# Optimization experiments

Hardware: AMD Instinct MI355X
Metric: run time of the kernel (lower is better)

Reference implementation:

```python
import jax, jax.numpy as jnp
import numpy as np

BETA = 1.0  # nn.SmoothL1Loss() default; module's self.beta=0.5 is never used


def smooth_l1(d):
    ad = jnp.abs(d)
    return jnp.where(ad < BETA, 0.5 * d * d / BETA, ad - 0.5 * BETA)


def setup_inputs() -> dict:
    key = jax.random.key(0)
    k1, k2, k3 = jax.random.split(key, 3)
    B, T, D = 32, 2048, 512
    preds = jax.random.normal(k1, (B, T, D), dtype=jnp.float32)
    targets = jax.random.normal(k2, (B, T, D), dtype=jnp.float32)
    # lengths in [1, T], sorted descending (pack_padded_sequence convention)
    decode_lengths = jnp.sort(jax.random.randint(k3, (B,), 1, T + 1))[::-1]
    return {"preds": preds, "targets": targets, "decode_lengths": decode_lengths}


def reference(preds, targets, decode_lengths):
    B, T, D = preds.shape
    mask = (jnp.arange(T)[None, :] < decode_lengths[:, None]).astype(preds.dtype)  # [B,T]
    lens = decode_lengths.astype(preds.dtype)[:, None]  # [B,1]

    # sentence loss: SmoothL1 between per-sample time-means, mean over D, summed over B
    pred_mean = jnp.einsum('btd,bt->bd', preds, mask) / lens
    targ_mean = jnp.einsum('btd,bt->bd', targets, mask) / lens
    sentence_loss = jnp.sum(jnp.mean(smooth_l1(pred_mean - targ_mean), axis=1))

    # word loss: SmoothL1 over all valid (packed) elements, mean reduction
    elem = smooth_l1(preds - targets) * mask[:, :, None]
    n_valid = jnp.sum(decode_lengths).astype(preds.dtype) * D
    word_loss = jnp.sum(elem) / n_valid

    return word_loss + sentence_loss / B
```

## Files before the change

kernel.cpp:

```cpp
#include <hip/hip_runtime.h>


#define BATCH 32
#define TLEN  2048
#define DDIM  512
#define ROWS  32
#define NCHUNK (TLEN / ROWS)
#define P1_THREADS 128

__device__ __forceinline__ float sl1(float d) {
    float ad = fabsf(d);
    return ad < 1.0f ? 0.5f * d * d : ad - 0.5f;
}

__global__ __launch_bounds__(P1_THREADS)
void pass1(const float* __restrict__ preds, const float* __restrict__ targs,
           const int* __restrict__ lens,
           float* __restrict__ partp,
           float* __restrict__ partt,
           float* __restrict__ wpart)
{
    const int b     = blockIdx.x;
    const int chunk = blockIdx.y;
    const int len   = lens[b];
    const int t0    = chunk * ROWS;
    if (t0 >= len) return;
    const int t1 = min(t0 + ROWS, len);

    const float4* __restrict__ p4 = (const float4*)(preds + (size_t)b * TLEN * DDIM);
    const float4* __restrict__ q4 = (const float4*)(targs + (size_t)b * TLEN * DDIM);
    const int lane4 = threadIdx.x;

    float4 sp = make_float4(0.f, 0.f, 0.f, 0.f);
    float4 st = make_float4(0.f, 0.f, 0.f, 0.f);
    float  w  = 0.f;

    for (int t = t0; t < t1; ++t) {
        float4 p = p4[(size_t)t * (DDIM / 4) + lane4];
        float4 q = q4[(size_t)t * (DDIM / 4) + lane4];
        sp.x += p.x; sp.y += p.y; sp.z += p.z; sp.w += p.w;
        st.x += q.x; st.y += q.y; st.z += q.z; st.w += q.w;
        w += sl1(p.x - q.x) + sl1(p.y - q.y) + sl1(p.z - q.z) + sl1(p.w - q.w);
    }

    float4* op = (float4*)(partp + ((size_t)b * NCHUNK + chunk) * DDIM);
    float4* ot = (float4*)(partt + ((size_t)b * NCHUNK + chunk) * DDIM);
    op[lane4] = sp;
    ot[lane4] = st;

    #pragma unroll
    for (int off = 32; off; off >>= 1) w += __shfl_down(w, off);
    __shared__ float ws[P1_THREADS / 64];
    if ((threadIdx.x & 63) == 0) ws[threadIdx.x >> 6] = w;
    __syncthreads();
    if (threadIdx.x == 0) wpart[b * NCHUNK + chunk] = ws[0] + ws[1];
}

__global__ __launch_bounds__(1024)
void pass2(const float* __restrict__ partp, const float* __restrict__ partt,
           const int* __restrict__ lens, const float* __restrict__ wpart,
           float* __restrict__ out)
{
    const int tid = threadIdx.x;

    float s = 0.f;
    for (int i = tid; i < BATCH * (DDIM / 4); i += 1024) {
        const int b   = i >> 7;
        const int d4  = i & 127;
        const int len = lens[b];
        const int nch = (len + ROWS - 1) / ROWS;
        const float4* pp = (const float4*)(partp + (size_t)b * NCHUNK * DDIM) + d4;
        const float4* tt = (const float4*)(partt + (size_t)b * NCHUNK * DDIM) + d4;
        float4 cp = make_float4(0.f, 0.f, 0.f, 0.f);
        float4 ct = make_float4(0.f, 0.f, 0.f, 0.f);
        for (int c = 0; c < nch; ++c) {
            float4 a  = pp[(size_t)c * (DDIM / 4)];
            float4 bb = tt[(size_t)c * (DDIM / 4)];
            cp.x += a.x; cp.y += a.y; cp.z += a.z; cp.w += a.w;
            ct.x += bb.x; ct.y += bb.y; ct.z += bb.z; ct.w += bb.w;
        }
        const float invL = 1.f / (float)len;
        s += sl1((cp.x - ct.x) * invL) + sl1((cp.y - ct.y) * invL)
           + sl1((cp.z - ct.z) * invL) + sl1((cp.w - ct.w) * invL);
    }

    float wsum = 0.f;
    for (int i = tid; i < BATCH * NCHUNK; i += 1024) {
        const int b = i >> 6;
        const int c = i & (NCHUNK - 1);
        if (c * ROWS < lens[b]) wsum += wpart[i];
    }

    #pragma unroll
    for (int off = 32; off; off >>= 1) {
        s    += __shfl_down(s, off);
        wsum += __shfl_down(wsum, off);
    }
    __shared__ float rs[16], rw[16];
    if ((tid & 63) == 0) { rs[tid >> 6] = s; rw[tid >> 6] = wsum; }
    __syncthreads();
    if (tid == 0) {
        float sent = 0.f, word = 0.f;
        #pragma unroll
        for (int i = 0; i < 16; ++i) { sent += rs[i]; word += rw[i]; }
        float nvalid = 0.f;
        for (int b = 0; b < BATCH; ++b) nvalid += (float)lens[b];
        out[0] = word / (nvalid * (float)DDIM)
               + sent / ((float)DDIM * (float)BATCH);
    }
}

extern "C" void kernel_launch(void* const* d_in, const int* in_sizes, int n_in,
                              void* d_out, int out_size, void* d_ws, size_t ws_size,
                              hipStream_t stream) {
    const float* preds = (const float*)d_in[0];
    const float* targs = (const float*)d_in[1];
    const int*   lens  = (const int*)d_in[2];
    float* out = (float*)d_out;

    float* partp = (float*)d_ws;
    float* partt = partp + (size_t)BATCH * NCHUNK * DDIM;
    float* wpart = partt + (size_t)BATCH * NCHUNK * DDIM;

    dim3 grid1(BATCH, NCHUNK);
    pass1<<<grid1, P1_THREADS, 0, stream>>>(preds, targs, lens, partp, partt, wpart);
    pass2<<<1, 1024, 0, stream>>>(partp, partt, lens, wpart, out);
}
```

Measured before the change: 291.5 us.

## Split second-pass reduction across batch blocks and add final tiny reduce kernel

The single-block 1024-thread second pass is replaced by a 32-block pass (one block per batch item) that reduces that item's chunk partials, followed by a one-wavefront third kernel that combines the per-batch results. This spreads the partial-sum reads across many CUs instead of one, removing a serial single-CU bottleneck. It costs an extra kernel launch and a small extra workspace write/read.

```diff
diff --git a/kernel.cpp b/kernel.cpp
--- a/kernel.cpp
+++ b/kernel.cpp
@@ -56,58 +56,64 @@
     if (threadIdx.x == 0) wpart[b * NCHUNK + chunk] = ws[0] + ws[1];
 }
 
-__global__ __launch_bounds__(1024)
+__global__ __launch_bounds__(128)
 void pass2(const float* __restrict__ partp, const float* __restrict__ partt,
            const int* __restrict__ lens, const float* __restrict__ wpart,
-           float* __restrict__ out)
+           float* __restrict__ sentb,
+           float* __restrict__ wordb)
 {
+    const int b   = blockIdx.x;
     const int tid = threadIdx.x;
+    const int len = lens[b];
+    const int nch = (len + ROWS - 1) / ROWS;
 
-    float s = 0.f;
-    for (int i = tid; i < BATCH * (DDIM / 4); i += 1024) {
-        const int b   = i >> 7;
-        const int d4  = i & 127;
-        const int len = lens[b];
-        const int nch = (len + ROWS - 1) / ROWS;
-        const float4* pp = (const float4*)(partp + (size_t)b * NCHUNK * DDIM) + d4;
-        const float4* tt = (const float4*)(partt + (size_t)b * NCHUNK * DDIM) + d4;
-        float4 cp = make_float4(0.f, 0.f, 0.f, 0.f);
-        float4 ct = make_float4(0.f, 0.f, 0.f, 0.f);
-        for (int c = 0; c < nch; ++c) {
-            float4 a  = pp[(size_t)c * (DDIM / 4)];
-            float4 bb = tt[(size_t)c * (DDIM / 4)];
-            cp.x += a.x; cp.y += a.y; cp.z += a.z; cp.w += a.w;
-            ct.x += bb.x; ct.y += bb.y; ct.z += bb.z; ct.w += bb.w;
-        }
-        const float invL = 1.f / (float)len;
-        s += sl1((cp.x - ct.x) * invL) + sl1((cp.y - ct.y) * invL)
-           + sl1((cp.z - ct.z) * invL) + sl1((cp.w - ct.w) * invL);
+    const float4* pp = (const float4*)(partp + (size_t)b * NCHUNK * DDIM) + tid;
+    const float4* tt = (const float4*)(partt + (size_t)b * NCHUNK * DDIM) + tid;
+    float4 cp = make_float4(0.f, 0.f, 0.f, 0.f);
+    float4 ct = make_float4(0.f, 0.f, 0.f, 0.f);
+    for (int c = 0; c < nch; ++c) {
+        float4 a = pp[(size_t)c * (DDIM / 4)];
+        float4 q = tt[(size_t)c * (DDIM / 4)];
+        cp.x += a.x; cp.y += a.y; cp.z += a.z; cp.w += a.w;
+        ct.x += q.x; ct.y += q.y; ct.z += q.z; ct.w += q.w;
     }
+    const float invL = 1.f / (float)len;
+    float s = sl1((cp.x - ct.x) * invL) + sl1((cp.y - ct.y) * invL)
+            + sl1((cp.z - ct.z) * invL) + sl1((cp.w - ct.w) * invL);
 
-    float wsum = 0.f;
-    for (int i = tid; i < BATCH * NCHUNK; i += 1024) {
-        const int b = i >> 6;
-        const int c = i & (NCHUNK - 1);
-        if (c * ROWS < lens[b]) wsum += wpart[i];
-    }
+    float w = 0.f;
+    for (int c = tid; c < nch; c += 128) w += wpart[b * NCHUNK + c];
 
     #pragma unroll
     for (int off = 32; off; off >>= 1) {
-        s    += __shfl_down(s, off);
-        wsum += __shfl_down(wsum, off);
+        s += __shfl_down(s, off);
+        w += __shfl_down(w, off);
     }
-    __shared__ float rs[16], rw[16];
-    if ((tid & 63) == 0) { rs[tid >> 6] = s; rw[tid >> 6] = wsum; }
+    __shared__ float rs[2], rw[2];
+    if ((tid & 63) == 0) { rs[tid >> 6] = s; rw[tid >> 6] = w; }
     __syncthreads();
-    if (tid == 0) {
-        float sent = 0.f, word = 0.f;
-        #pragma unroll
-        for (int i = 0; i < 16; ++i) { sent += rs[i]; word += rw[i]; }
-        float nvalid = 0.f;
-        for (int b = 0; b < BATCH; ++b) nvalid += (float)lens[b];
-        out[0] = word / (nvalid * (float)DDIM)
-               + sent / ((float)DDIM * (float)BATCH);
+    if (tid == 0) { sentb[b] = rs[0] + rs[1]; wordb[b] = rw[0] + rw[1]; }
+}
+
+__global__ __launch_bounds__(64)
+void pass3(const float* __restrict__ sentb, const float* __restrict__ wordb,
+           const int* __restrict__ lens, float* __restrict__ out)
+{
+    const int tid = threadIdx.x;
+    float s = 0.f, w = 0.f, n = 0.f;
+    if (tid < BATCH) {
+        s = sentb[tid];
+        w = wordb[tid];
+        n = (float)lens[tid];
     }
+    #pragma unroll
+    for (int off = 32; off; off >>= 1) {
+        s += __shfl_down(s, off);
+        w += __shfl_down(w, off);
+        n += __shfl_down(n, off);
+    }
+    if (tid == 0)
+        out[0] = w / (n * (float)DDIM) + s / ((float)DDIM * (float)BATCH);
 }
 
 extern "C" void kernel_launch(void* const* d_in, const int* in_sizes, int n_in,
@@ -121,8 +127,11 @@
     float* partp = (float*)d_ws;
     float* partt = partp + (size_t)BATCH * NCHUNK * DDIM;
     float* wpart = partt + (size_t)BATCH * NCHUNK * DDIM;
+    float* sentb = wpart + BATCH * NCHUNK;
+    float* wordb = sentb + BATCH;
 
     dim3 grid1(BATCH, NCHUNK);
     pass1<<<grid1, P1_THREADS, 0, stream>>>(preds, targs, lens, partp, partt, wpart);
-    pass2<<<1, 1024, 0, stream>>>(partp, partt, lens, wpart, out);
+    pass2<<<BATCH, 128, 0, stream>>>(partp, partt, lens, wpart, sentb, wordb);
+    pass3<<<1, 64, 0, stream>>>(sentb, wordb, lens, out);
 }
```

New measurement: 262.2 us. 10.0% less time.
